# Optimization experiments

Hardware: AMD Instinct MI355X
Metric: run time of the kernel (lower is better)

The kernel has to match this reference:

```python
import jax, jax.numpy as jnp
import numpy as np

N_HEAD = 16
NEG_INF = jnp.float32(-1e30)


def setup_inputs() -> dict:
    key = jax.random.key(0)
    k1, k2, k3 = jax.random.split(key, 3)
    B, T, C = 2, 2048, 1024
    x = jax.random.normal(k1, (B, T, C), dtype=jnp.float32)
    attn_mask = jnp.ones((B, T), dtype=jnp.int32)
    W_qkv = jax.random.normal(k2, (C, 3 * C), dtype=jnp.float32) * (1.0 / np.sqrt(C))
    b_qkv = jnp.zeros((3 * C,), dtype=jnp.float32)
    W_proj = jax.random.normal(k3, (C, C), dtype=jnp.float32) * (1.0 / np.sqrt(C))
    b_proj = jnp.zeros((C,), dtype=jnp.float32)
    return {"x": x, "attn_mask": attn_mask, "W_qkv": W_qkv, "b_qkv": b_qkv,
            "W_proj": W_proj, "b_proj": b_proj}


def reference(x, attn_mask, W_qkv, b_qkv, W_proj, b_proj):
    B, T, C = x.shape
    H = N_HEAD
    hd = C // H
    qkv = x @ W_qkv + b_qkv                       # [B,T,3C]
    q, k, v = jnp.split(qkv, 3, axis=-1)
    q = q.reshape(B, T, H, hd).transpose(0, 2, 1, 3)  # [B,H,T,hd]
    k = k.reshape(B, T, H, hd).transpose(0, 2, 1, 3)
    v = v.reshape(B, T, H, hd).transpose(0, 2, 1, 3)
    att = jnp.einsum('bhqd,bhkd->bhqk', q, k) / jnp.float32(np.sqrt(hd))  # [B,H,T,T]
    causal = jnp.tril(jnp.ones((T, T), dtype=bool))[None, None]           # [1,1,T,T]
    pad = (attn_mask != 0)[:, None, None, :]                              # [B,1,1,T]
    att = jnp.where(causal & pad, att, NEG_INF)
    att = jax.nn.softmax(att, axis=-1)
    y = jnp.einsum('bhqk,bhkd->bhqd', att, v)     # [B,H,T,hd]
    y = y.transpose(0, 2, 1, 3).reshape(B, T, C)
    return y @ W_proj + b_proj
```

## Files before the change

### kernel.cpp

```cpp
#include <hip/hip_runtime.h>

#define T_SEQ 2048
#define NHEAD 16
#define HD 64
#define CDIM 1024

typedef __bf16 bf16x8 __attribute__((ext_vector_type(8)));
typedef float f32x4 __attribute__((ext_vector_type(4)));
typedef float f32x16 __attribute__((ext_vector_type(16)));

union U16x8 { uint4 u4; unsigned short s[8]; bf16x8 b; };

__device__ __forceinline__ float bf2f(unsigned short u) {
    return __uint_as_float(((unsigned int)u) << 16);
}
__device__ __forceinline__ unsigned short f2bf(float f) {
    unsigned int u = __float_as_uint(f);
    u += 0x7fffu + ((u >> 16) & 1u);
    return (unsigned short)(u >> 16);
}
__device__ __forceinline__ U16x8 load8f(const float* __restrict__ p) {
    U16x8 r;
    float4 f0 = *(const float4*)p;
    float4 f1 = *(const float4*)(p + 4);
    r.s[0] = f2bf(f0.x); r.s[1] = f2bf(f0.y); r.s[2] = f2bf(f0.z); r.s[3] = f2bf(f0.w);
    r.s[4] = f2bf(f1.x); r.s[5] = f2bf(f1.y); r.s[6] = f2bf(f1.z); r.s[7] = f2bf(f1.w);
    return r;
}

__device__ __forceinline__ void async_copy16(const unsigned short* g, unsigned short* l) {
    __builtin_amdgcn_global_load_lds(
        (const __attribute__((address_space(1))) unsigned int*)g,
        (__attribute__((address_space(3))) unsigned int*)l, 16, 0, 0);
}

#define LOG2E 1.442695040f

#define BAR()    asm volatile("s_barrier" ::: "memory")
#define LGKM0()  asm volatile("s_waitcnt lgkmcnt(0)" ::: "memory")
#define VMC6()   asm volatile("s_waitcnt vmcnt(6)" ::: "memory")
#define VMC0()   asm volatile("s_waitcnt vmcnt(0)" ::: "memory")

__device__ __forceinline__ unsigned int cvtpk_bf16(float lo, float hi) {
    unsigned int r;
    asm("v_cvt_pk_bf16_f32 %0, %1, %2" : "=v"(r) : "v"(lo), "v"(hi));
    return r;
}
__device__ __forceinline__ void plane32swap(unsigned int &x, unsigned int &y) {
    asm("v_permlane32_swap_b32 %0, %1" : "+v"(x), "+v"(y));
}

__global__ __launch_bounds__(256) void conv_bf16(
    const float* __restrict__ in, unsigned short* __restrict__ out, int n)
{
    const int i = (blockIdx.x * 256 + threadIdx.x) * 8;
    if (i < n) {
        U16x8 o = load8f(&in[i]);
        *(uint4*)&out[i] = o.u4;
    }
}

__global__ __launch_bounds__(256) void transpose_conv(
    const float* __restrict__ in, unsigned short* __restrict__ out, int R, int C)
{
    __shared__ float tile[64][65];
    const int r0 = blockIdx.x * 64;
    const int c0 = blockIdx.y * 64;
    const int tid = threadIdx.x;
    const int rr = tid >> 4;
    const int cc = (tid & 15) * 4;
#pragma unroll
    for (int p = 0; p < 4; ++p) {
        float4 v = *(const float4*)&in[(size_t)(r0 + p * 16 + rr) * C + c0 + cc];
        tile[p * 16 + rr][cc] = v.x;
        tile[p * 16 + rr][cc + 1] = v.y;
        tile[p * 16 + rr][cc + 2] = v.z;
        tile[p * 16 + rr][cc + 3] = v.w;
    }
    __syncthreads();
    const int n = tid >> 2;
    const int s = (tid & 3) * 8;
#pragma unroll
    for (int p = 0; p < 2; ++p) {
        const int k = s + p * 32;
        U16x8 o;
#pragma unroll
        for (int j = 0; j < 8; ++j) o.s[j] = f2bf(tile[k + j][n]);
        *(uint4*)&out[(size_t)(c0 + n) * R + r0 + k] = o.u4;
    }
}

__device__ __forceinline__ void gemm128_core(
    const unsigned short* __restrict__ A,
    const unsigned short* __restrict__ Bt,
    int K, int m0, int n0,
    unsigned short* As, unsigned short* Bs, f32x4 acc[4][4])
{
    const int tid = threadIdx.x;
    const int w = tid >> 6, lane = tid & 63;
    const int ln = lane & 15, quad = lane >> 4;
    const int wm = w >> 1, wn = w & 1;
    const int lr = lane >> 3;
    const int lc = (lane & 7) * 8;

    for (int kb = 0; kb < K; kb += 64) {
        __syncthreads();
#pragma unroll
        for (int i = 0; i < 4; ++i) {
            async_copy16(&A[(size_t)(m0 + w * 32 + i * 8 + lr) * K + kb + lc],
                         &As[(w * 32 + i * 8) * 64]);
            async_copy16(&Bt[(size_t)(n0 + w * 32 + i * 8 + lr) * K + kb + lc],
                         &Bs[(w * 32 + i * 8) * 64]);
        }
        __syncthreads();
#pragma unroll
        for (int kk = 0; kk < 2; ++kk) {
            U16x8 af[4], bff[4];
#pragma unroll
            for (int i = 0; i < 4; ++i)
                af[i].u4 = *(const uint4*)&As[(wm * 64 + i * 16 + ln) * 64 + kk * 32 + quad * 8];
#pragma unroll
            for (int j = 0; j < 4; ++j)
                bff[j].u4 = *(const uint4*)&Bs[(wn * 64 + j * 16 + ln) * 64 + kk * 32 + quad * 8];
#pragma unroll
            for (int i = 0; i < 4; ++i)
#pragma unroll
                for (int j = 0; j < 4; ++j)
                    acc[i][j] = __builtin_amdgcn_mfma_f32_16x16x32_bf16(af[i].b, bff[j].b, acc[i][j], 0, 0, 0);
        }
    }
}

__device__ __forceinline__ void stageA(const unsigned short* __restrict__ A,
                                       unsigned short* buf,
                                       int m0, int t, int unit, int w, int lane)
{
#pragma unroll
    for (int s = 0; s < 2; ++s) {
        const int r0 = s * 128 + unit * 64 + w * 8;
        const int row = r0 + (lane >> 3);
        const int col = (16 * (lane & 7)) ^ ((row & 4) ? 32 : 0);
        const unsigned short* src = A + (size_t)(m0 + row) * CDIM + t * 64 + (col >> 1);
        async_copy16(src, buf + r0 * 64);
    }
}

__device__ __forceinline__ void stageB(const unsigned short* __restrict__ B,
                                       unsigned short* buf,
                                       int n0, int t, int unit, int w, int lane)
{
#pragma unroll
    for (int s = 0; s < 2; ++s) {
        const int slice = s * 8 + w;
        const int r0 = (slice >> 2) * 64 + unit * 32 + (slice & 3) * 8;
        const int row = r0 + (lane >> 3);
        const int col = (16 * (lane & 7)) ^ ((row & 4) ? 32 : 0);
        const unsigned short* src = B + (size_t)(n0 + row) * CDIM + t * 64 + (col >> 1);
        async_copy16(src, buf + r0 * 64);
    }
}

__device__ __forceinline__ void readA(U16x8 af[4][2], const unsigned short* buf,
                                      int wm, int qm, int ln, int quad)
{
#pragma unroll
    for (int i = 0; i < 4; ++i) {
        const int row = wm * 128 + qm * 64 + i * 16 + ln;
        const int sw = (row & 4) ? 32 : 0;
#pragma unroll
        for (int kk = 0; kk < 2; ++kk) {
            const int byt = row * 128 + ((kk * 64 + quad * 16) ^ sw);
            af[i][kk].u4 = *(const uint4*)((const char*)buf + byt);
        }
    }
}

__device__ __forceinline__ void readB(U16x8 bf[2][2], const unsigned short* buf,
                                      int wn, int qn, int ln, int quad)
{
#pragma unroll
    for (int jj = 0; jj < 2; ++jj) {
        const int row = wn * 64 + qn * 32 + jj * 16 + ln;
        const int sw = (row & 4) ? 32 : 0;
#pragma unroll
        for (int kk = 0; kk < 2; ++kk) {
            const int byt = row * 128 + ((kk * 64 + quad * 16) ^ sw);
            bf[jj][kk].u4 = *(const uint4*)((const char*)buf + byt);
        }
    }
}

template<int QM, int QN>
__device__ __forceinline__ void mfma16(f32x4 acc[8][4], const U16x8 af[4][2],
                                       const U16x8 bf[2][2])
{
    __builtin_amdgcn_s_setprio(1);
#pragma unroll
    for (int i = 0; i < 4; ++i)
#pragma unroll
        for (int jj = 0; jj < 2; ++jj)
#pragma unroll
            for (int kk = 0; kk < 2; ++kk)
                acc[QM * 4 + i][QN * 2 + jj] = __builtin_amdgcn_mfma_f32_16x16x32_bf16(
                    af[i][kk].b, bf[jj][kk].b, acc[QM * 4 + i][QN * 2 + jj], 0, 0, 0);
    __builtin_amdgcn_s_setprio(0);
}

__global__ __launch_bounds__(512) void qkv8(
    const unsigned short* __restrict__ Xb,
    const unsigned short* __restrict__ Wt,
    const float* __restrict__ bias,
    unsigned short* __restrict__ Qp,
    unsigned short* __restrict__ Kp,
    unsigned short* __restrict__ Vtp)
{
    __shared__ __align__(1024) unsigned short smem[4][16384];
    unsigned short* Ab0 = smem[0];
    unsigned short* Ab1 = smem[1];
    unsigned short* Bb0 = smem[2];
    unsigned short* Bb1 = smem[3];

    const int tid = threadIdx.x;
    const int w = tid >> 6, lane = tid & 63;
    const int ln = lane & 15, quad = lane >> 4;
    const int wm = w >> 2, wn = w & 3;

    const int bid = blockIdx.x;
    const int swz = (bid & 7) * 24 + (bid >> 3);
    const int nt = swz % 12, mt = swz / 12;
    const int m0 = mt * 256, n0 = nt * 256;

    f32x4 acc[8][4];
#pragma unroll
    for (int i = 0; i < 8; ++i)
#pragma unroll
        for (int j = 0; j < 4; ++j) acc[i][j] = (f32x4){0.f, 0.f, 0.f, 0.f};

    stageA(Xb, Ab0, m0, 0, 0, w, lane);
    stageB(Wt, Bb0, n0, 0, 0, w, lane);
    stageB(Wt, Bb0, n0, 0, 1, w, lane);
    stageA(Xb, Ab0, m0, 0, 1, w, lane);
    stageA(Xb, Ab1, m0, 1, 0, w, lane);
    stageB(Wt, Bb1, n0, 1, 0, w, lane);
    stageB(Wt, Bb1, n0, 1, 1, w, lane);
    VMC6();
    BAR();

    U16x8 af[4][2], bq0[2][2], bq1[2][2];

    for (int j = 0; j < 7; ++j) {
        const int e = 2 * j, o = 2 * j + 1;
        readA(af, Ab0, wm, 0, ln, quad);
        readB(bq0, Bb0, wn, 0, ln, quad);
        stageA(Xb, Ab1, m0, o, 1, w, lane);
        BAR(); LGKM0();
        mfma16<0, 0>(acc, af, bq0);
        LGKM0(); BAR();
        readB(bq1, Bb0, wn, 1, ln, quad);
        stageA(Xb, Ab0, m0, e + 2, 0, w, lane);
        BAR(); LGKM0();
        mfma16<0, 1>(acc, af, bq1);
        LGKM0(); BAR();
        readA(af, Ab0, wm, 1, ln, quad);
        stageB(Wt, Bb0, n0, e + 2, 0, w, lane);
        BAR(); LGKM0();
        mfma16<1, 0>(acc, af, bq0);
        LGKM0(); BAR();
        stageB(Wt, Bb0, n0, e + 2, 1, w, lane);
        BAR();
        mfma16<1, 1>(acc, af, bq1);
        VMC6(); BAR();
        readA(af, Ab1, wm, 0, ln, quad);
        readB(bq0, Bb1, wn, 0, ln, quad);
        stageA(Xb, Ab0, m0, e + 2, 1, w, lane);
        BAR(); LGKM0();
        mfma16<0, 0>(acc, af, bq0);
        LGKM0(); BAR();
        readB(bq1, Bb1, wn, 1, ln, quad);
        stageA(Xb, Ab1, m0, o + 2, 0, w, lane);
        BAR(); LGKM0();
        mfma16<0, 1>(acc, af, bq1);
        LGKM0(); BAR();
        readA(af, Ab1, wm, 1, ln, quad);
        stageB(Wt, Bb1, n0, o + 2, 0, w, lane);
        BAR(); LGKM0();
        mfma16<1, 0>(acc, af, bq0);
        LGKM0(); BAR();
        stageB(Wt, Bb1, n0, o + 2, 1, w, lane);
        BAR();
        mfma16<1, 1>(acc, af, bq1);
        VMC6(); BAR();
    }

    stageA(Xb, Ab1, m0, 15, 1, w, lane);
    VMC0(); BAR();

    readA(af, Ab0, wm, 0, ln, quad);
    readB(bq0, Bb0, wn, 0, ln, quad);
    readB(bq1, Bb0, wn, 1, ln, quad);
    mfma16<0, 0>(acc, af, bq0);
    mfma16<0, 1>(acc, af, bq1);
    readA(af, Ab0, wm, 1, ln, quad);
    mfma16<1, 0>(acc, af, bq0);
    mfma16<1, 1>(acc, af, bq1);

    readA(af, Ab1, wm, 0, ln, quad);
    readB(bq0, Bb1, wn, 0, ln, quad);
    readB(bq1, Bb1, wn, 1, ln, quad);
    mfma16<0, 0>(acc, af, bq0);
    mfma16<0, 1>(acc, af, bq1);
    readA(af, Ab1, wm, 1, ln, quad);
    mfma16<1, 0>(acc, af, bq0);
    mfma16<1, 1>(acc, af, bq1);

    const int which = n0 >> 10;
    float bv[4];
#pragma unroll
    for (int jj = 0; jj < 4; ++jj) bv[jj] = bias[n0 + wn * 64 + jj * 16 + ln];

    if (which < 2) {
        unsigned short* dst = (which == 0) ? Qp : Kp;
#pragma unroll
        for (int jj = 0; jj < 4; ++jj) {
            const int n = n0 + wn * 64 + jj * 16 + ln;
            const int h = (n >> 6) & 15, d = n & 63;
#pragma unroll
            for (int i = 0; i < 8; ++i)
#pragma unroll
                for (int r = 0; r < 4; ++r) {
                    const int m = m0 + wm * 128 + i * 16 + quad * 4 + r;
                    const int b = m >> 11, tt = m & 2047;
                    dst[(((size_t)(b * NHEAD + h) * T_SEQ) + tt) * HD + d] =
                        f2bf(acc[i][jj][r] + bv[jj]);
                }
        }
    } else {
#pragma unroll
        for (int jj = 0; jj < 4; ++jj) {
            const int n = n0 + wn * 64 + jj * 16 + ln;
            const int c = n - 2048;
#pragma unroll
            for (int i = 0; i < 8; ++i) {
                const int m00 = m0 + wm * 128 + i * 16 + quad * 4;
                const int b = m00 >> 11, tt = m00 & 2047;
                ushort4 pk;
                pk.x = f2bf(acc[i][jj][0] + bv[jj]);
                pk.y = f2bf(acc[i][jj][1] + bv[jj]);
                pk.z = f2bf(acc[i][jj][2] + bv[jj]);
                pk.w = f2bf(acc[i][jj][3] + bv[jj]);
                *(ushort4*)&Vtp[(size_t)(b * 1024 + c) * T_SEQ + tt] = pk;
            }
        }
    }
}

__global__ __launch_bounds__(256) void proj_gemm(
    const unsigned short* __restrict__ Yin,
    const unsigned short* __restrict__ Wt,
    const float* __restrict__ bias,
    float* __restrict__ out)
{
    __shared__ unsigned short As[128 * 64];
    __shared__ unsigned short Bs[128 * 64];
    const int m0 = blockIdx.y * 128;
    const int n0 = blockIdx.x * 128;

    f32x4 acc[4][4];
#pragma unroll
    for (int i = 0; i < 4; ++i)
#pragma unroll
        for (int j = 0; j < 4; ++j) acc[i][j] = (f32x4){0.f, 0.f, 0.f, 0.f};

    gemm128_core(Yin, Wt, CDIM, m0, n0, As, Bs, acc);

    const int tid = threadIdx.x;
    const int w = tid >> 6, lane = tid & 63;
    const int ln = lane & 15, quad = lane >> 4;
    const int wm = w >> 1, wn = w & 1;

#pragma unroll
    for (int j = 0; j < 4; ++j) {
        const int n = n0 + wn * 64 + j * 16 + ln;
        const float bv = bias[n];
#pragma unroll
        for (int i = 0; i < 4; ++i)
#pragma unroll
            for (int r = 0; r < 4; ++r) {
                const int m = m0 + wm * 64 + i * 16 + quad * 4 + r;
                out[(size_t)m * CDIM + n] = acc[i][j][r] + bv;
            }
    }
}


#define FW_LOADSET(S, t)                                                              \
    {                                                                                 \
        const int _r = (t) * 32 + l31;                                                \
        k##S[0].u4 = *(const uint4*)&Kb[(size_t)_r * HD + hi * 8];                    \
        k##S[1].u4 = *(const uint4*)&Kb[(size_t)_r * HD + 16 + hi * 8];               \
        k##S[2].u4 = *(const uint4*)&Kb[(size_t)_r * HD + 32 + hi * 8];               \
        k##S[3].u4 = *(const uint4*)&Kb[(size_t)_r * HD + 48 + hi * 8];               \
        v##S[0].u4 = *(const uint4*)&Vb[(size_t)l31 * T_SEQ + (t) * 32 + hi * 8];     \
        v##S[1].u4 = *(const uint4*)&Vb[(size_t)l31 * T_SEQ + (t) * 32 + 16 + hi * 8];\
        v##S[2].u4 = *(const uint4*)&Vb[(size_t)(l31 + 32) * T_SEQ + (t) * 32 + hi * 8];\
        v##S[3].u4 = *(const uint4*)&Vb[(size_t)(l31 + 32) * T_SEQ + (t) * 32 + 16 + hi * 8];\
        m##S = mrow[(t) * 32 + l31];                                                  \
    }

#define FW_BODY(S, kb)                                                                \
    {                                                                                 \
        const bool allv = (__ballot(m##S != 0) == 0xFFFFFFFFFFFFFFFFull);             \
        f32x16 sc;                                                                    \
        _Pragma("unroll")                                                             \
        for (int r = 0; r < 16; ++r) sc[r] = 0.f;                                     \
        __builtin_amdgcn_s_setprio(1);                                                \
        sc = __builtin_amdgcn_mfma_f32_32x32x16_bf16(k##S[0].b, qf[0].b, sc, 0, 0, 0);\
        sc = __builtin_amdgcn_mfma_f32_32x32x16_bf16(k##S[1].b, qf[1].b, sc, 0, 0, 0);\
        sc = __builtin_amdgcn_mfma_f32_32x32x16_bf16(k##S[2].b, qf[2].b, sc, 0, 0, 0);\
        sc = __builtin_amdgcn_mfma_f32_32x32x16_bf16(k##S[3].b, qf[3].b, sc, 0, 0, 0);\
        __builtin_amdgcn_s_setprio(0);                                                \
        if (allv) {                                                                   \
            _Pragma("unroll")                                                         \
            for (int r = 0; r < 16; ++r) sc[r] *= 0.125f;                             \
        } else {                                                                      \
            const float mv0 = m##S ? 0.f : -1.0e30f;                                  \
            _Pragma("unroll")                                                         \
            for (int r = 0; r < 16; ++r)                                              \
                sc[r] = fmaf(sc[r], 0.125f,                                           \
                             __shfl(mv0, (r & 3) + 8 * (r >> 2) + 4 * hi));           \
        }                                                                             \
        if ((kb) == c) {                                                              \
            _Pragma("unroll")                                                         \
            for (int r = 0; r < 16; ++r)                                              \
                if ((r & 3) + 8 * (r >> 2) + 4 * hi > l31) sc[r] = -1.0e30f;          \
        }                                                                             \
        float tm = -3.0e38f;                                                          \
        _Pragma("unroll")                                                             \
        for (int r = 0; r < 16; ++r) tm = fmaxf(tm, sc[r]);                           \
        tm = fmaxf(tm, __shfl_xor(tm, 32));                                           \
        if (__any(tm > m_r + 8.f)) {                                                  \
            const float mn = fmaxf(m_r, tm);                                          \
            const float a = __builtin_amdgcn_exp2f((m_r - mn) * LOG2E);               \
            m_r = mn; mL = mn * LOG2E;                                                \
            l_r *= a;                                                                 \
            _Pragma("unroll")                                                         \
            for (int r = 0; r < 16; ++r) {                                            \
                const float ar = __shfl(a, (r & 3) + 8 * (r >> 2) + 4 * hi);          \
                oA0[r] *= ar; oA1[r] *= ar;                                           \
            }                                                                         \
        }                                                                             \
        float ps = 0.f;                                                               \
        _Pragma("unroll")                                                             \
        for (int r = 0; r < 16; ++r) {                                                \
            const float p = __builtin_amdgcn_exp2f(fmaf(sc[r], LOG2E, -mL));          \
            sc[r] = p; ps += p;                                                       \
        }                                                                             \
        l_r += ps;                                                                    \
        unsigned int x0, y0, x1, y1;                                                  \
        U16x8 pa0, pa1;                                                               \
        x0 = cvtpk_bf16(sc[0], sc[1]); x1 = cvtpk_bf16(sc[2], sc[3]);                 \
        y0 = cvtpk_bf16(sc[4], sc[5]); y1 = cvtpk_bf16(sc[6], sc[7]);                 \
        plane32swap(x0, y0); plane32swap(x1, y1);                                     \
        pa0.u4 = make_uint4(x0, x1, y0, y1);                                          \
        x0 = cvtpk_bf16(sc[8], sc[9]);  x1 = cvtpk_bf16(sc[10], sc[11]);              \
        y0 = cvtpk_bf16(sc[12], sc[13]); y1 = cvtpk_bf16(sc[14], sc[15]);             \
        plane32swap(x0, y0); plane32swap(x1, y1);                                     \
        pa1.u4 = make_uint4(x0, x1, y0, y1);                                          \
        __builtin_amdgcn_s_setprio(1);                                                \
        oA0 = __builtin_amdgcn_mfma_f32_32x32x16_bf16(pa0.b, v##S[0].b, oA0, 0, 0, 0);\
        oA0 = __builtin_amdgcn_mfma_f32_32x32x16_bf16(pa1.b, v##S[1].b, oA0, 0, 0, 0);\
        oA1 = __builtin_amdgcn_mfma_f32_32x32x16_bf16(pa0.b, v##S[2].b, oA1, 0, 0, 0);\
        oA1 = __builtin_amdgcn_mfma_f32_32x32x16_bf16(pa1.b, v##S[3].b, oA1, 0, 0, 0);\
        __builtin_amdgcn_s_setprio(0);                                                \
    }

__global__ __launch_bounds__(256, 2) void flash_warp(
    const unsigned short* __restrict__ Qp,
    const unsigned short* __restrict__ Kp,
    const unsigned short* __restrict__ Vtp,
    const int* __restrict__ mask,
    unsigned short* __restrict__ Y)
{
    const int bid = blockIdx.x;
    const int tid = threadIdx.x;
    const int w = tid >> 6, lane = tid & 63;
    const int l31 = lane & 31, hi = lane >> 5;

    const int bh = (bid & 7) + 8 * w;
    const int b = bh >> 4, h = bh & 15;
    const int c = 63 - (bid >> 3);
    const int q0 = c * 32;
    const size_t base = (size_t)bh * T_SEQ * HD;

    const unsigned short* Kb = Kp + base;
    const unsigned short* Vb = Vtp + base;
    const int* mrow = mask + b * T_SEQ;

    U16x8 qf[4];
    {
        const unsigned short* qrow = &Qp[base + (size_t)(q0 + l31) * HD];
#pragma unroll
        for (int c4 = 0; c4 < 4; ++c4)
            qf[c4].u4 = *(const uint4*)&qrow[c4 * 16 + hi * 8];
    }

    f32x16 oA0, oA1;
#pragma unroll
    for (int r = 0; r < 16; ++r) { oA0[r] = 0.f; oA1[r] = 0.f; }
    float m_r = -3.0e38f, mL = 0.f, l_r = 0.f;

    U16x8 kA[4], vA[4], kB[4], vB[4];
    int mA, mB;

    FW_LOADSET(A, 0);
    int kb = 0;
    while (true) {
        if (kb < c) FW_LOADSET(B, kb + 1);
        FW_BODY(A, kb);
        ++kb; if (kb > c) break;
        if (kb < c) FW_LOADSET(A, kb + 1);
        FW_BODY(B, kb);
        ++kb; if (kb > c) break;
    }

    const float lt = l_r + __shfl_xor(l_r, 32);
    const float inv = 1.0f / lt;
#pragma unroll
    for (int r = 0; r < 16; ++r) {
        const int crow = (r & 3) + 8 * (r >> 2) + 4 * hi;
        const float ir = __shfl(inv, crow);
        const size_t row = (size_t)(b * T_SEQ + q0 + crow);
        Y[row * CDIM + h * HD + l31]      = f2bf(oA0[r] * ir);
        Y[row * CDIM + h * HD + 32 + l31] = f2bf(oA1[r] * ir);
    }
}

extern "C" void kernel_launch(void* const* d_in, const int* in_sizes, int n_in,
                              void* d_out, int out_size, void* d_ws, size_t ws_size,
                              hipStream_t stream)
{
    const float* X     = (const float*)d_in[0];
    const int*   mask  = (const int*)d_in[1];
    const float* Wqkv  = (const float*)d_in[2];
    const float* bqkv  = (const float*)d_in[3];
    const float* Wproj = (const float*)d_in[4];
    const float* bproj = (const float*)d_in[5];
    float* out = (float*)d_out;

    const size_t per = (size_t)2 * NHEAD * T_SEQ * HD;
    unsigned short* Qp     = (unsigned short*)d_ws;
    unsigned short* Kp     = Qp + per;
    unsigned short* Vtp    = Kp + per;
    unsigned short* Xb     = Vtp + per;
    unsigned short* Yp     = Xb;
    unsigned short* Wqkvt  = Xb + per;
    unsigned short* Wprojt = Wqkvt + (size_t)3 * CDIM * CDIM;

    conv_bf16<<<2048, 256, 0, stream>>>(X, Xb, 4 * 1024 * 1024);
    transpose_conv<<<dim3(16, 48), 256, 0, stream>>>(Wqkv, Wqkvt, CDIM, 3 * CDIM);
    transpose_conv<<<dim3(16, 16), 256, 0, stream>>>(Wproj, Wprojt, CDIM, CDIM);

    qkv8<<<192, 512, 0, stream>>>(Xb, Wqkvt, bqkv, Qp, Kp, Vtp);
    flash_warp<<<512, 256, 0, stream>>>(Qp, Kp, Vtp, mask, Yp);
    proj_gemm<<<dim3(8, 32), 256, 0, stream>>>(Yp, Wprojt, bproj, out);
}
```

Baseline: 251.5 us.

## Split KV range across warps with LDS softmax merge and paired causal query tiles

Restructures the attention kernel so each block handles one head and a pair of 32-row query tiles (c and 63-c), with the four warps striding over key blocks and merging their partial softmax state (max, sum, output) through shared memory. This replaces the one-warp-per-query-tile scheme, aiming to balance causal work across blocks and cut per-warp serial loop length. V loads move into the body (no double buffering for V) to reduce register use and allow 4 blocks per CU. It adds LDS traffic, two barriers per pass, and a cross-warp reduction epilogue.

```diff
diff --git a/kernel.cpp b/kernel.cpp
--- a/kernel.cpp
+++ b/kernel.cpp
@@ -393,22 +393,22 @@
 }
 
 
-#define FW_LOADSET(S, t)                                                              \
+#define FW_LOADK(S, t)                                                                \
     {                                                                                 \
         const int _r = (t) * 32 + l31;                                                \
         k##S[0].u4 = *(const uint4*)&Kb[(size_t)_r * HD + hi * 8];                    \
         k##S[1].u4 = *(const uint4*)&Kb[(size_t)_r * HD + 16 + hi * 8];               \
         k##S[2].u4 = *(const uint4*)&Kb[(size_t)_r * HD + 32 + hi * 8];               \
         k##S[3].u4 = *(const uint4*)&Kb[(size_t)_r * HD + 48 + hi * 8];               \
-        v##S[0].u4 = *(const uint4*)&Vb[(size_t)l31 * T_SEQ + (t) * 32 + hi * 8];     \
-        v##S[1].u4 = *(const uint4*)&Vb[(size_t)l31 * T_SEQ + (t) * 32 + 16 + hi * 8];\
-        v##S[2].u4 = *(const uint4*)&Vb[(size_t)(l31 + 32) * T_SEQ + (t) * 32 + hi * 8];\
-        v##S[3].u4 = *(const uint4*)&Vb[(size_t)(l31 + 32) * T_SEQ + (t) * 32 + 16 + hi * 8];\
         m##S = mrow[(t) * 32 + l31];                                                  \
     }
 
 #define FW_BODY(S, kb)                                                                \
     {                                                                                 \
+        vC[0].u4 = *(const uint4*)&Vb[(size_t)l31 * T_SEQ + (kb) * 32 + hi * 8];      \
+        vC[1].u4 = *(const uint4*)&Vb[(size_t)l31 * T_SEQ + (kb) * 32 + 16 + hi * 8]; \
+        vC[2].u4 = *(const uint4*)&Vb[(size_t)(l31 + 32) * T_SEQ + (kb) * 32 + hi * 8];\
+        vC[3].u4 = *(const uint4*)&Vb[(size_t)(l31 + 32) * T_SEQ + (kb) * 32 + 16 + hi * 8];\
         const bool allv = (__ballot(m##S != 0) == 0xFFFFFFFFFFFFFFFFull);             \
         f32x16 sc;                                                                    \
         _Pragma("unroll")                                                             \
@@ -467,71 +467,110 @@
         plane32swap(x0, y0); plane32swap(x1, y1);                                     \
         pa1.u4 = make_uint4(x0, x1, y0, y1);                                          \
         __builtin_amdgcn_s_setprio(1);                                                \
-        oA0 = __builtin_amdgcn_mfma_f32_32x32x16_bf16(pa0.b, v##S[0].b, oA0, 0, 0, 0);\
-        oA0 = __builtin_amdgcn_mfma_f32_32x32x16_bf16(pa1.b, v##S[1].b, oA0, 0, 0, 0);\
-        oA1 = __builtin_amdgcn_mfma_f32_32x32x16_bf16(pa0.b, v##S[2].b, oA1, 0, 0, 0);\
-        oA1 = __builtin_amdgcn_mfma_f32_32x32x16_bf16(pa1.b, v##S[3].b, oA1, 0, 0, 0);\
+        oA0 = __builtin_amdgcn_mfma_f32_32x32x16_bf16(pa0.b, vC[0].b, oA0, 0, 0, 0);  \
+        oA0 = __builtin_amdgcn_mfma_f32_32x32x16_bf16(pa1.b, vC[1].b, oA0, 0, 0, 0);  \
+        oA1 = __builtin_amdgcn_mfma_f32_32x32x16_bf16(pa0.b, vC[2].b, oA1, 0, 0, 0);  \
+        oA1 = __builtin_amdgcn_mfma_f32_32x32x16_bf16(pa1.b, vC[3].b, oA1, 0, 0, 0);  \
         __builtin_amdgcn_s_setprio(0);                                                \
     }
 
-__global__ __launch_bounds__(256, 2) void flash_warp(
+__global__ __launch_bounds__(256, 4) void flash_pair(
     const unsigned short* __restrict__ Qp,
     const unsigned short* __restrict__ Kp,
     const unsigned short* __restrict__ Vtp,
     const int* __restrict__ mask,
     unsigned short* __restrict__ Y)
 {
+    __shared__ __align__(16) float Os[4][32][68];
+    __shared__ float mls[4][2][32];
+
     const int bid = blockIdx.x;
+    const int bh = bid & 31;
+    const int pair = bid >> 5;
+    const int b = bh >> 4, h = bh & 15;
     const int tid = threadIdx.x;
     const int w = tid >> 6, lane = tid & 63;
     const int l31 = lane & 31, hi = lane >> 5;
-
-    const int bh = (bid & 7) + 8 * w;
-    const int b = bh >> 4, h = bh & 15;
-    const int c = 63 - (bid >> 3);
-    const int q0 = c * 32;
     const size_t base = (size_t)bh * T_SEQ * HD;
 
     const unsigned short* Kb = Kp + base;
     const unsigned short* Vb = Vtp + base;
     const int* mrow = mask + b * T_SEQ;
 
-    U16x8 qf[4];
-    {
-        const unsigned short* qrow = &Qp[base + (size_t)(q0 + l31) * HD];
-#pragma unroll
-        for (int c4 = 0; c4 < 4; ++c4)
-            qf[c4].u4 = *(const uint4*)&qrow[c4 * 16 + hi * 8];
-    }
-
-    f32x16 oA0, oA1;
-#pragma unroll
-    for (int r = 0; r < 16; ++r) { oA0[r] = 0.f; oA1[r] = 0.f; }
-    float m_r = -3.0e38f, mL = 0.f, l_r = 0.f;
-
-    U16x8 kA[4], vA[4], kB[4], vB[4];
-    int mA, mB;
-
-    FW_LOADSET(A, 0);
-    int kb = 0;
-    while (true) {
-        if (kb < c) FW_LOADSET(B, kb + 1);
-        FW_BODY(A, kb);
-        ++kb; if (kb > c) break;
-        if (kb < c) FW_LOADSET(A, kb + 1);
-        FW_BODY(B, kb);
-        ++kb; if (kb > c) break;
-    }
-
-    const float lt = l_r + __shfl_xor(l_r, 32);
-    const float inv = 1.0f / lt;
-#pragma unroll
-    for (int r = 0; r < 16; ++r) {
-        const int crow = (r & 3) + 8 * (r >> 2) + 4 * hi;
-        const float ir = __shfl(inv, crow);
-        const size_t row = (size_t)(b * T_SEQ + q0 + crow);
-        Y[row * CDIM + h * HD + l31]      = f2bf(oA0[r] * ir);
-        Y[row * CDIM + h * HD + 32 + l31] = f2bf(oA1[r] * ir);
+#pragma unroll 1
+    for (int pass = 0; pass < 2; ++pass) {
+        const int c = pass ? (63 - pair) : pair;
+        const int q0 = c * 32;
+
+        U16x8 qf[4];
+        {
+            const unsigned short* qrow = &Qp[base + (size_t)(q0 + l31) * HD];
+#pragma unroll
+            for (int c4 = 0; c4 < 4; ++c4)
+                qf[c4].u4 = *(const uint4*)&qrow[c4 * 16 + hi * 8];
+        }
+
+        f32x16 oA0, oA1;
+#pragma unroll
+        for (int r = 0; r < 16; ++r) { oA0[r] = 0.f; oA1[r] = 0.f; }
+        float m_r = -3.0e38f, mL = 0.f, l_r = 0.f;
+
+        U16x8 kA[4], kB[4], vC[4];
+        int mA, mB;
+
+        int t = w;
+        if (t <= c) {
+            FW_LOADK(A, t);
+            while (true) {
+                if (t + 4 <= c) FW_LOADK(B, t + 4);
+                FW_BODY(A, t);
+                t += 4; if (t > c) break;
+                if (t + 4 <= c) FW_LOADK(A, t + 4);
+                FW_BODY(B, t);
+                t += 4; if (t > c) break;
+            }
+        }
+
+        l_r += __shfl_xor(l_r, 32);
+
+        if (hi == 0) { mls[w][0][l31] = m_r; mls[w][1][l31] = l_r; }
+#pragma unroll
+        for (int r = 0; r < 16; ++r) {
+            const int crow = (r & 3) + 8 * (r >> 2) + 4 * hi;
+            Os[w][crow][l31]      = oA0[r];
+            Os[w][crow][32 + l31] = oA1[r];
+        }
+        __syncthreads();
+
+        {
+            const int q = tid >> 3, d0 = (tid & 7) * 8;
+            const float m0v = mls[0][0][q], m1v = mls[1][0][q];
+            const float m2v = mls[2][0][q], m3v = mls[3][0][q];
+            const float M = fmaxf(fmaxf(m0v, m1v), fmaxf(m2v, m3v));
+            const float f0 = __builtin_amdgcn_exp2f((m0v - M) * LOG2E);
+            const float f1 = __builtin_amdgcn_exp2f((m1v - M) * LOG2E);
+            const float f2 = __builtin_amdgcn_exp2f((m2v - M) * LOG2E);
+            const float f3 = __builtin_amdgcn_exp2f((m3v - M) * LOG2E);
+            const float L = f0 * mls[0][1][q] + f1 * mls[1][1][q]
+                          + f2 * mls[2][1][q] + f3 * mls[3][1][q];
+            const float inv = 1.0f / L;
+            unsigned short* yp = &Y[(size_t)(b * T_SEQ + q0 + q) * CDIM + h * HD + d0];
+#pragma unroll
+            for (int half = 0; half < 2; ++half) {
+                f32x4 a0 = *(const f32x4*)&Os[0][q][d0 + half * 4];
+                f32x4 a1 = *(const f32x4*)&Os[1][q][d0 + half * 4];
+                f32x4 a2 = *(const f32x4*)&Os[2][q][d0 + half * 4];
+                f32x4 a3 = *(const f32x4*)&Os[3][q][d0 + half * 4];
+                ushort4 pk;
+                float v0 = (f0 * a0[0] + f1 * a1[0] + f2 * a2[0] + f3 * a3[0]) * inv;
+                float v1 = (f0 * a0[1] + f1 * a1[1] + f2 * a2[1] + f3 * a3[1]) * inv;
+                float v2 = (f0 * a0[2] + f1 * a1[2] + f2 * a2[2] + f3 * a3[2]) * inv;
+                float v3 = (f0 * a0[3] + f1 * a1[3] + f2 * a2[3] + f3 * a3[3]) * inv;
+                pk.x = f2bf(v0); pk.y = f2bf(v1); pk.z = f2bf(v2); pk.w = f2bf(v3);
+                *(ushort4*)&yp[half * 4] = pk;
+            }
+        }
+        __syncthreads();
     }
 }
 
@@ -561,6 +600,6 @@
     transpose_conv<<<dim3(16, 16), 256, 0, stream>>>(Wproj, Wprojt, CDIM, CDIM);
 
     qkv8<<<192, 512, 0, stream>>>(Xb, Wqkvt, bqkv, Qp, Kp, Vtp);
-    flash_warp<<<512, 256, 0, stream>>>(Qp, Kp, Vtp, mask, Yp);
+    flash_pair<<<1024, 256, 0, stream>>>(Qp, Kp, Vtp, mask, Yp);
     proj_gemm<<<dim3(8, 32), 256, 0, stream>>>(Yp, Wprojt, bproj, out);
 }
```

Result: slower. 263.7 us (+4.9%).
